# Optimization experiments

Hardware: AMD Instinct MI355X
Metric: run time of the kernel (lower is better)

The kernel has to match this reference:

```python
import jax, jax.numpy as jnp
import numpy as np

T = 1000      # self.length in DMM
B = 16384     # batch
Z_DIM, X_DIM, H_DIM = 2, 3, 2
SIGMA = 0.01  # fixed scale used in both model and guide Normals
LOG2PI = float(np.log(2.0 * np.pi))


def _normal_logprob(x, mu, sigma):
    # elementwise Normal(mu, sigma).log_prob(x)
    return -0.5 * jnp.square((x - mu) / sigma) - jnp.log(sigma) - 0.5 * LOG2PI


def setup_inputs() -> dict:
    key = jax.random.key(0)
    ks = jax.random.split(key, 12)
    s = 0.3  # modest init scale for tiny linears
    return {
        "data": jax.random.normal(ks[0], (T, B, X_DIM), dtype=jnp.float32),
        "eps":  jax.random.normal(ks[1], (T, B, Z_DIM), dtype=jnp.float32),
        # guide RNN (Elman, tanh): input 3 -> hidden 2
        "W_ih": jax.random.normal(ks[2], (H_DIM, X_DIM), dtype=jnp.float32) * s,
        "W_hh": jax.random.normal(ks[3], (H_DIM, H_DIM), dtype=jnp.float32) * s,
        "b_ih": jax.random.normal(ks[4], (H_DIM,), dtype=jnp.float32) * s,
        "b_hh": jax.random.normal(ks[5], (H_DIM,), dtype=jnp.float32) * s,
        "h0":   jnp.zeros((H_DIM,), dtype=jnp.float32),   # nn.Parameter h_0
        "z0":   jnp.zeros((Z_DIM,), dtype=jnp.float32),   # nn.Parameter z_0
        # transition: Linear(2,2)
        "Wt": jax.random.normal(ks[6], (Z_DIM, Z_DIM), dtype=jnp.float32) * s,
        "bt": jax.random.normal(ks[7], (Z_DIM,), dtype=jnp.float32) * s,
        # emission: Linear(2,3)
        "We": jax.random.normal(ks[8], (X_DIM, Z_DIM), dtype=jnp.float32) * s,
        "be": jax.random.normal(ks[9], (X_DIM,), dtype=jnp.float32) * s,
    }


def reference(data, eps, W_ih, W_hh, b_ih, b_hh, h0, z0, Wt, bt, We, be):
    """Guide RNN + reparameterized latents + model log-joint minus guide log-prob.

    data: [T, B, 3], eps: [T, B, 2]. Returns scalar ELBO-style objective.
    """
    batch = data.shape[1]

    # --- guide: RNN over data (sequential recurrence, lax.scan) ---
    def step(h, x_t):
        h_new = jnp.tanh(x_t @ W_ih.T + b_ih + h @ W_hh.T + b_hh)
        return h_new, h_new

    h0b = jnp.broadcast_to(h0, (batch, H_DIM))
    _, rnn_out = jax.lax.scan(step, h0b, data)            # [T, B, 2]

    # z_t = Normal(rnn_out[t-1], SIGMA) sample, t = 1..T-1 (reparameterized)
    q_loc = rnn_out[:-1]                                   # [T-1, B, 2]
    z = q_loc + SIGMA * eps[1:]                            # [T-1, B, 2]

    # --- model: transition + emission over the latent chain ---
    z_prev = jnp.concatenate(
        [jnp.broadcast_to(z0, (1, batch, Z_DIM)), z[:-1]], axis=0)  # [T-1, B, 2]
    z_loc = z_prev @ Wt.T + bt                             # transition mean
    x_loc = z @ We.T + be                                  # emission mean [T-1, B, 3]

    logp = (_normal_logprob(z, z_loc, SIGMA).sum()
            + _normal_logprob(data[1:], x_loc, SIGMA).sum())
    logq = _normal_logprob(z, q_loc, SIGMA).sum()
    return logp - logq
```

## Files before the change

kernel.cpp:

```cpp
#include <hip/hip_runtime.h>

#define T_STEPS 1000
#define BATCH   16384

#define NCHUNK  20
#define CHUNK_L (T_STEPS / NCHUNK)
#define WARMUP  32

__device__ __forceinline__ float fast_tanh(float x) {
    float e = __expf(2.0f * x);
    return 1.0f - __fdividef(2.0f, e + 1.0f);
}

__global__ __launch_bounds__(64)
void elbo_kernel(const float* __restrict__ data,
                 const float* __restrict__ eps,
                 const float* __restrict__ W_ih,
                 const float* __restrict__ W_hh,
                 const float* __restrict__ b_ih,
                 const float* __restrict__ b_hh,
                 const float* __restrict__ h0p,
                 const float* __restrict__ z0p,
                 const float* __restrict__ Wt,
                 const float* __restrict__ bt,
                 const float* __restrict__ We,
                 const float* __restrict__ be,
                 float* __restrict__ out)
{
    const int b  = blockIdx.x * 64 + threadIdx.x;
    const int c  = blockIdx.y;
    const int t0 = c * CHUNK_L;

    const float w00 = W_ih[0], w01 = W_ih[1], w02 = W_ih[2];
    const float w10 = W_ih[3], w11 = W_ih[4], w12 = W_ih[5];
    const float u00 = W_hh[0], u01 = W_hh[1];
    const float u10 = W_hh[2], u11 = W_hh[3];
    const float bs0 = b_ih[0] + b_hh[0];
    const float bs1 = b_ih[1] + b_hh[1];
    const float wt00 = Wt[0], wt01 = Wt[1], wt10 = Wt[2], wt11 = Wt[3];
    const float bt0 = bt[0], bt1 = bt[1];
    const float we00 = We[0], we01 = We[1];
    const float we10 = We[2], we11 = We[3];
    const float we20 = We[4], we21 = We[5];
    const float be0 = be[0], be1 = be[1], be2 = be[2];

    const size_t  dstride = (size_t)BATCH * 3;
    const float*  pd = data + (size_t)b * 3;
    const float2* pe = reinterpret_cast<const float2*>(eps) + b;

    float h0 = h0p[0], h1 = h0p[1];
    float zp0 = z0p[0], zp1 = z0p[1];

#define RNN_STEP(X0_, X1_, X2_)                                            \
    do {                                                                   \
        float p0_ = bs0;                                                   \
        p0_ = __fmaf_rn(w00, (X0_), p0_);                                  \
        p0_ = __fmaf_rn(w01, (X1_), p0_);                                  \
        p0_ = __fmaf_rn(w02, (X2_), p0_);                                  \
        p0_ = __fmaf_rn(u00, h0, p0_);                                     \
        p0_ = __fmaf_rn(u01, h1, p0_);                                     \
        float p1_ = bs1;                                                   \
        p1_ = __fmaf_rn(w10, (X0_), p1_);                                  \
        p1_ = __fmaf_rn(w11, (X1_), p1_);                                  \
        p1_ = __fmaf_rn(w12, (X2_), p1_);                                  \
        p1_ = __fmaf_rn(u10, h0, p1_);                                     \
        p1_ = __fmaf_rn(u11, h1, p1_);                                     \
        h0 = fast_tanh(p0_);                                               \
        h1 = fast_tanh(p1_);                                               \
    } while (0)

    if (c == 0) {
        const float* p = pd;
        RNN_STEP(p[0], p[1], p[2]);
    } else {
        const float* p = pd + (size_t)(t0 - 1 - WARMUP) * dstride;
#pragma unroll 4
        for (int k = 0; k < WARMUP; ++k) {
            const float X0 = p[0], X1 = p[1], X2 = p[2];
            p += dstride;
            RNN_STEP(X0, X1, X2);
        }
        {
            const float X0 = p[0], X1 = p[1], X2 = p[2];
            const float2 E = pe[(size_t)(t0 - 1) * BATCH];
            zp0 = __fmaf_rn(0.01f, E.x, h0);
            zp1 = __fmaf_rn(0.01f, E.y, h1);
            RNN_STEP(X0, X1, X2);
        }
    }

    const int   tm = (c == 0) ? 1 : t0;
    const int   na = (c == 0) ? (CHUNK_L - 1) : CHUNK_L;
    const float* px = pd + (size_t)tm * dstride;
    const float2* pq = pe + (size_t)tm * BATCH;

    float ssq = 0.0f;
    float esq = 0.0f;

#pragma unroll 5
    for (int k = 0; k < na; ++k) {
        const float X0 = px[0], X1 = px[1], X2 = px[2];
        const float2 E = *pq;
        px += dstride;
        pq += BATCH;

        const float z0 = __fmaf_rn(0.01f, E.x, h0);
        const float z1 = __fmaf_rn(0.01f, E.y, h1);
        const float zl0 = __fmaf_rn(wt00, zp0, __fmaf_rn(wt01, zp1, bt0));
        const float zl1 = __fmaf_rn(wt10, zp0, __fmaf_rn(wt11, zp1, bt1));
        const float xl0 = __fmaf_rn(we00, z0, __fmaf_rn(we01, z1, be0));
        const float xl1 = __fmaf_rn(we10, z0, __fmaf_rn(we11, z1, be1));
        const float xl2 = __fmaf_rn(we20, z0, __fmaf_rn(we21, z1, be2));
        const float r0 = z0 - zl0;
        const float r1 = z1 - zl1;
        const float r2 = X0 - xl0;
        const float r3 = X1 - xl1;
        const float r4 = X2 - xl2;
        float s = r0 * r0;
        s = __fmaf_rn(r1, r1, s);
        s = __fmaf_rn(r2, r2, s);
        s = __fmaf_rn(r3, r3, s);
        s = __fmaf_rn(r4, r4, s);
        ssq += s;
        esq = __fmaf_rn(E.x, E.x, esq);
        esq = __fmaf_rn(E.y, E.y, esq);
        zp0 = z0; zp1 = z1;

        RNN_STEP(X0, X1, X2);
    }
#undef RNN_STEP

    const float CPT = (float)na * (3.0f * 3.6862316527806026f);
    float tval = __fmaf_rn(ssq, -5000.0f, __fmaf_rn(esq, 0.5f, CPT));

#pragma unroll
    for (int off = 32; off >= 1; off >>= 1)
        tval += __shfl_down(tval, off, 64);

    if (threadIdx.x == 0)
        atomicAdd(out, tval);
}

extern "C" void kernel_launch(void* const* d_in, const int* in_sizes, int n_in,
                              void* d_out, int out_size, void* d_ws, size_t ws_size,
                              hipStream_t stream) {
    const float* data = (const float*)d_in[0];
    const float* eps  = (const float*)d_in[1];
    const float* W_ih = (const float*)d_in[2];
    const float* W_hh = (const float*)d_in[3];
    const float* b_ih = (const float*)d_in[4];
    const float* b_hh = (const float*)d_in[5];
    const float* h0   = (const float*)d_in[6];
    const float* z0   = (const float*)d_in[7];
    const float* Wt   = (const float*)d_in[8];
    const float* bt   = (const float*)d_in[9];
    const float* We   = (const float*)d_in[10];
    const float* be   = (const float*)d_in[11];
    float* out = (float*)d_out;

    hipMemsetAsync(out, 0, sizeof(float), stream);
    elbo_kernel<<<dim3(BATCH / 64, NCHUNK), dim3(64), 0, stream>>>(
        data, eps, W_ih, W_hh, b_ih, b_hh, h0, z0, Wt, bt, We, be, out);
}
```

Measured before the change: 425.2 us.

## Software-prefetch timesteps into registers and replace atomics with partial-sum reduction

Restructures the per-chunk time loop so each thread keeps a ring of several timesteps of data and eps in registers, issuing each load well ahead of its use to hide memory latency. Chunking changes to 25 chunks of 40 steps with a 20-step warmup, which cuts redundant warmup work. The global atomicAdd and memset are replaced by per-block partial sums in workspace plus a second single-block reduction kernel. The shorter warmup may change accuracy slightly, the register ring raises register pressure, and the extra launch adds a small fixed cost.

```diff
diff --git a/kernel.cpp b/kernel.cpp
--- a/kernel.cpp
+++ b/kernel.cpp
@@ -3,13 +3,112 @@
 #define T_STEPS 1000
 #define BATCH   16384
 
-#define NCHUNK  20
-#define CHUNK_L (T_STEPS / NCHUNK)
-#define WARMUP  32
+#define CH      40
+#define NCHUNK  25
+#define WARM    20
+#define PF      8
+#define PFW     5
+#define NPART   (NCHUNK * (BATCH / 64))
+
+struct P {
+    float w00,w01,w02,w10,w11,w12;
+    float u00,u01,u10,u11,bs0,bs1;
+    float wt00,wt01,wt10,wt11,bt0,bt1;
+    float we00,we01,we10,we11,we20,we21,be0,be1,be2;
+};
 
 __device__ __forceinline__ float fast_tanh(float x) {
     float e = __expf(2.0f * x);
     return 1.0f - __fdividef(2.0f, e + 1.0f);
+}
+
+__device__ __forceinline__ void rnn_step(const P& p, float X0, float X1, float X2,
+                                         float& h0, float& h1) {
+    float p0 = p.bs0;
+    p0 = __fmaf_rn(p.w00, X0, p0);
+    p0 = __fmaf_rn(p.w01, X1, p0);
+    p0 = __fmaf_rn(p.w02, X2, p0);
+    p0 = __fmaf_rn(p.u00, h0, p0);
+    p0 = __fmaf_rn(p.u01, h1, p0);
+    float p1 = p.bs1;
+    p1 = __fmaf_rn(p.w10, X0, p1);
+    p1 = __fmaf_rn(p.w11, X1, p1);
+    p1 = __fmaf_rn(p.w12, X2, p1);
+    p1 = __fmaf_rn(p.u10, h0, p1);
+    p1 = __fmaf_rn(p.u11, h1, p1);
+    h0 = fast_tanh(p0);
+    h1 = fast_tanh(p1);
+}
+
+__device__ __forceinline__ void body(const P& p, float X0, float X1, float X2,
+                                     float E0, float E1,
+                                     float& h0, float& h1, float& zp0, float& zp1,
+                                     float& ssq, float& esq) {
+    const float z0 = __fmaf_rn(0.01f, E0, h0);
+    const float z1 = __fmaf_rn(0.01f, E1, h1);
+    const float zl0 = __fmaf_rn(p.wt00, zp0, __fmaf_rn(p.wt01, zp1, p.bt0));
+    const float zl1 = __fmaf_rn(p.wt10, zp0, __fmaf_rn(p.wt11, zp1, p.bt1));
+    const float xl0 = __fmaf_rn(p.we00, z0, __fmaf_rn(p.we01, z1, p.be0));
+    const float xl1 = __fmaf_rn(p.we10, z0, __fmaf_rn(p.we11, z1, p.be1));
+    const float xl2 = __fmaf_rn(p.we20, z0, __fmaf_rn(p.we21, z1, p.be2));
+    const float r0 = z0 - zl0;
+    const float r1 = z1 - zl1;
+    const float r2 = X0 - xl0;
+    const float r3 = X1 - xl1;
+    const float r4 = X2 - xl2;
+    float s = r0 * r0;
+    s = __fmaf_rn(r1, r1, s);
+    s = __fmaf_rn(r2, r2, s);
+    s = __fmaf_rn(r3, r3, s);
+    s = __fmaf_rn(r4, r4, s);
+    ssq += s;
+    esq = __fmaf_rn(E0, E0, esq);
+    esq = __fmaf_rn(E1, E1, esq);
+    zp0 = z0; zp1 = z1;
+    rnn_step(p, X0, X1, X2, h0, h1);
+}
+
+template<int NA>
+__device__ __forceinline__ void main_phase(const P& p,
+        const float* __restrict__ px, const float2* __restrict__ pq,
+        float& h0, float& h1, float& zp0, float& zp1,
+        float& ssq, float& esq) {
+    const size_t dstr = (size_t)BATCH * 3;
+    float x0[PF], x1[PF], x2[PF], e0[PF], e1[PF];
+#pragma unroll
+    for (int i = 0; i < PF; ++i) {
+        x0[i] = px[0]; x1[i] = px[1]; x2[i] = px[2]; px += dstr;
+        float2 E = *pq; pq += BATCH;
+        e0[i] = E.x; e1[i] = E.y;
+    }
+    constexpr int S   = (NA - PF) / PF;
+    constexpr int REM = NA - PF - S * PF;
+#pragma unroll
+    for (int k = 0; k < S; ++k) {
+#pragma unroll
+        for (int i = 0; i < PF; ++i) {
+            const float X0 = x0[i], X1 = x1[i], X2 = x2[i];
+            const float E0 = e0[i], E1 = e1[i];
+            x0[i] = px[0]; x1[i] = px[1]; x2[i] = px[2]; px += dstr;
+            float2 E = *pq; pq += BATCH;
+            e0[i] = E.x; e1[i] = E.y;
+            body(p, X0, X1, X2, E0, E1, h0, h1, zp0, zp1, ssq, esq);
+        }
+    }
+#pragma unroll
+    for (int i = 0; i < PF; ++i) {
+        const float X0 = x0[i], X1 = x1[i], X2 = x2[i];
+        const float E0 = e0[i], E1 = e1[i];
+        if (i < REM) {
+            x0[i] = px[0]; x1[i] = px[1]; x2[i] = px[2]; px += dstr;
+            float2 E = *pq; pq += BATCH;
+            e0[i] = E.x; e1[i] = E.y;
+        }
+        body(p, X0, X1, X2, E0, E1, h0, h1, zp0, zp1, ssq, esq);
+    }
+#pragma unroll
+    for (int i = 0; i < REM; ++i)
+        body(p, x0[i], x1[i], x2[i], e0[i], e1[i], h0, h1, zp0, zp1, ssq, esq);
 }
 
 __global__ __launch_bounds__(64)
@@ -25,111 +124,75 @@
                  const float* __restrict__ bt,
                  const float* __restrict__ We,
                  const float* __restrict__ be,
-                 float* __restrict__ out)
+                 float* __restrict__ partial)
 {
-    const int b  = blockIdx.x * 64 + threadIdx.x;
-    const int c  = blockIdx.y;
-    const int t0 = c * CHUNK_L;
-
-    const float w00 = W_ih[0], w01 = W_ih[1], w02 = W_ih[2];
-    const float w10 = W_ih[3], w11 = W_ih[4], w12 = W_ih[5];
-    const float u00 = W_hh[0], u01 = W_hh[1];
-    const float u10 = W_hh[2], u11 = W_hh[3];
-    const float bs0 = b_ih[0] + b_hh[0];
-    const float bs1 = b_ih[1] + b_hh[1];
-    const float wt00 = Wt[0], wt01 = Wt[1], wt10 = Wt[2], wt11 = Wt[3];
-    const float bt0 = bt[0], bt1 = bt[1];
-    const float we00 = We[0], we01 = We[1];
-    const float we10 = We[2], we11 = We[3];
-    const float we20 = We[4], we21 = We[5];
-    const float be0 = be[0], be1 = be[1], be2 = be[2];
-
-    const size_t  dstride = (size_t)BATCH * 3;
+    const int b = blockIdx.x * 64 + threadIdx.x;
+    const int c = blockIdx.y;
+    const int t0 = c * CH + 1;
+
+    P p;
+    p.w00 = W_ih[0]; p.w01 = W_ih[1]; p.w02 = W_ih[2];
+    p.w10 = W_ih[3]; p.w11 = W_ih[4]; p.w12 = W_ih[5];
+    p.u00 = W_hh[0]; p.u01 = W_hh[1]; p.u10 = W_hh[2]; p.u11 = W_hh[3];
+    p.bs0 = b_ih[0] + b_hh[0];
+    p.bs1 = b_ih[1] + b_hh[1];
+    p.wt00 = Wt[0]; p.wt01 = Wt[1]; p.wt10 = Wt[2]; p.wt11 = Wt[3];
+    p.bt0 = bt[0]; p.bt1 = bt[1];
+    p.we00 = We[0]; p.we01 = We[1];
+    p.we10 = We[2]; p.we11 = We[3];
+    p.we20 = We[4]; p.we21 = We[5];
+    p.be0 = be[0]; p.be1 = be[1]; p.be2 = be[2];
+
+    const size_t dstr = (size_t)BATCH * 3;
     const float*  pd = data + (size_t)b * 3;
     const float2* pe = reinterpret_cast<const float2*>(eps) + b;
 
     float h0 = h0p[0], h1 = h0p[1];
     float zp0 = z0p[0], zp1 = z0p[1];
-
-#define RNN_STEP(X0_, X1_, X2_)                                            \
-    do {                                                                   \
-        float p0_ = bs0;                                                   \
-        p0_ = __fmaf_rn(w00, (X0_), p0_);                                  \
-        p0_ = __fmaf_rn(w01, (X1_), p0_);                                  \
-        p0_ = __fmaf_rn(w02, (X2_), p0_);                                  \
-        p0_ = __fmaf_rn(u00, h0, p0_);                                     \
-        p0_ = __fmaf_rn(u01, h1, p0_);                                     \
-        float p1_ = bs1;                                                   \
-        p1_ = __fmaf_rn(w10, (X0_), p1_);                                  \
-        p1_ = __fmaf_rn(w11, (X1_), p1_);                                  \
-        p1_ = __fmaf_rn(w12, (X2_), p1_);                                  \
-        p1_ = __fmaf_rn(u10, h0, p1_);                                     \
-        p1_ = __fmaf_rn(u11, h1, p1_);                                     \
-        h0 = fast_tanh(p0_);                                               \
-        h1 = fast_tanh(p1_);                                               \
-    } while (0)
-
-    if (c == 0) {
-        const float* p = pd;
-        RNN_STEP(p[0], p[1], p[2]);
+    float ssq = 0.0f, esq = 0.0f;
+
+    const float*  px;
+    const float2* pq;
+
+    if (c > 0) {
+        const float* pw = pd + (size_t)(t0 - 1 - WARM) * dstr;
+        float y0[PFW], y1[PFW], y2[PFW];
+#pragma unroll
+        for (int i = 0; i < PFW; ++i) {
+            y0[i] = pw[0]; y1[i] = pw[1]; y2[i] = pw[2]; pw += dstr;
+        }
+#pragma unroll
+        for (int k = 0; k < (WARM - PFW) / PFW; ++k) {
+#pragma unroll
+            for (int i = 0; i < PFW; ++i) {
+                const float X0 = y0[i], X1 = y1[i], X2 = y2[i];
+                y0[i] = pw[0]; y1[i] = pw[1]; y2[i] = pw[2]; pw += dstr;
+                rnn_step(p, X0, X1, X2, h0, h1);
+            }
+        }
+#pragma unroll
+        for (int i = 0; i < PFW; ++i)
+            rnn_step(p, y0[i], y1[i], y2[i], h0, h1);
+        const float X0 = pw[0], X1 = pw[1], X2 = pw[2];
+        const float2* pq1 = pe + (size_t)(t0 - 1) * BATCH;
+        const float2 E = *pq1;
+        zp0 = __fmaf_rn(0.01f, E.x, h0);
+        zp1 = __fmaf_rn(0.01f, E.y, h1);
+        rnn_step(p, X0, X1, X2, h0, h1);
+        px = pw + dstr;
+        pq = pq1 + BATCH;
     } else {
-        const float* p = pd + (size_t)(t0 - 1 - WARMUP) * dstride;
-#pragma unroll 4
-        for (int k = 0; k < WARMUP; ++k) {
-            const float X0 = p[0], X1 = p[1], X2 = p[2];
-            p += dstride;
-            RNN_STEP(X0, X1, X2);
-        }
-        {
-            const float X0 = p[0], X1 = p[1], X2 = p[2];
-            const float2 E = pe[(size_t)(t0 - 1) * BATCH];
-            zp0 = __fmaf_rn(0.01f, E.x, h0);
-            zp1 = __fmaf_rn(0.01f, E.y, h1);
-            RNN_STEP(X0, X1, X2);
-        }
-    }
-
-    const int   tm = (c == 0) ? 1 : t0;
-    const int   na = (c == 0) ? (CHUNK_L - 1) : CHUNK_L;
-    const float* px = pd + (size_t)tm * dstride;
-    const float2* pq = pe + (size_t)tm * BATCH;
-
-    float ssq = 0.0f;
-    float esq = 0.0f;
-
-#pragma unroll 5
-    for (int k = 0; k < na; ++k) {
-        const float X0 = px[0], X1 = px[1], X2 = px[2];
-        const float2 E = *pq;
-        px += dstride;
-        pq += BATCH;
-
-        const float z0 = __fmaf_rn(0.01f, E.x, h0);
-        const float z1 = __fmaf_rn(0.01f, E.y, h1);
-        const float zl0 = __fmaf_rn(wt00, zp0, __fmaf_rn(wt01, zp1, bt0));
-        const float zl1 = __fmaf_rn(wt10, zp0, __fmaf_rn(wt11, zp1, bt1));
-        const float xl0 = __fmaf_rn(we00, z0, __fmaf_rn(we01, z1, be0));
-        const float xl1 = __fmaf_rn(we10, z0, __fmaf_rn(we11, z1, be1));
-        const float xl2 = __fmaf_rn(we20, z0, __fmaf_rn(we21, z1, be2));
-        const float r0 = z0 - zl0;
-        const float r1 = z1 - zl1;
-        const float r2 = X0 - xl0;
-        const float r3 = X1 - xl1;
-        const float r4 = X2 - xl2;
-        float s = r0 * r0;
-        s = __fmaf_rn(r1, r1, s);
-        s = __fmaf_rn(r2, r2, s);
-        s = __fmaf_rn(r3, r3, s);
-        s = __fmaf_rn(r4, r4, s);
-        ssq += s;
-        esq = __fmaf_rn(E.x, E.x, esq);
-        esq = __fmaf_rn(E.y, E.y, esq);
-        zp0 = z0; zp1 = z1;
-
-        RNN_STEP(X0, X1, X2);
-    }
-#undef RNN_STEP
-
+        rnn_step(p, pd[0], pd[1], pd[2], h0, h1);
+        px = pd + dstr;
+        pq = pe + BATCH;
+    }
+
+    if (c < NCHUNK - 1)
+        main_phase<CH>(p, px, pq, h0, h1, zp0, zp1, ssq, esq);
+    else
+        main_phase<T_STEPS - 1 - (NCHUNK - 1) * CH>(p, px, pq, h0, h1, zp0, zp1, ssq, esq);
+
+    const int na = (c < NCHUNK - 1) ? CH : (T_STEPS - 1 - (NCHUNK - 1) * CH);
     const float CPT = (float)na * (3.0f * 3.6862316527806026f);
     float tval = __fmaf_rn(ssq, -5000.0f, __fmaf_rn(esq, 0.5f, CPT));
 
@@ -138,7 +201,23 @@
         tval += __shfl_down(tval, off, 64);
 
     if (threadIdx.x == 0)
-        atomicAdd(out, tval);
+        partial[c * (BATCH / 64) + blockIdx.x] = tval;
+}
+
+__global__ __launch_bounds__(256)
+void reduce_kernel(const float* __restrict__ partial, float* __restrict__ out)
+{
+    float s = 0.0f;
+    for (int i = threadIdx.x; i < NPART; i += 256)
+        s += partial[i];
+    __shared__ float sm[4];
+#pragma unroll
+    for (int off = 32; off >= 1; off >>= 1)
+        s += __shfl_down(s, off, 64);
+    if ((threadIdx.x & 63) == 0) sm[threadIdx.x >> 6] = s;
+    __syncthreads();
+    if (threadIdx.x == 0)
+        out[0] = sm[0] + sm[1] + sm[2] + sm[3];
 }
 
 extern "C" void kernel_launch(void* const* d_in, const int* in_sizes, int n_in,
@@ -156,9 +235,10 @@
     const float* bt   = (const float*)d_in[9];
     const float* We   = (const float*)d_in[10];
     const float* be   = (const float*)d_in[11];
-    float* out = (float*)d_out;
-
-    hipMemsetAsync(out, 0, sizeof(float), stream);
+    float* out     = (float*)d_out;
+    float* partial = (float*)d_ws;
+
     elbo_kernel<<<dim3(BATCH / 64, NCHUNK), dim3(64), 0, stream>>>(
-        data, eps, W_ih, W_hh, b_ih, b_hh, h0, z0, Wt, bt, We, be, out);
-}
+        data, eps, W_ih, W_hh, b_ih, b_hh, h0, z0, Wt, bt, We, be, partial);
+    reduce_kernel<<<dim3(1), dim3(256), 0, stream>>>(partial, out);
+}
```

Result: faster. 385.8 us (-9.3%).
